# Kernel tuning notes

Measured on AMD Instinct MI355X. Metric: run time of the kernel, lower is better.

## Reference

```python
import jax, jax.numpy as jnp
import numpy as np

B_AUDIOS = 64      # num audios in batch
NODES    = 2048    # 5-frame chunks (nodes) per audio
IN, HID, OUT = 512, 256, 128
HEADS, NCLS  = 2, 7
NEG_SLOPE = 0.2    # PyG GATConv default


def setup_inputs() -> dict:
    key = jax.random.key(0)
    ks = jax.random.split(key, 12)
    N = B_AUDIOS * NODES
    # chain edges within each audio: i -> i+1 (local), offset per audio
    base = np.arange(NODES - 1)
    src = (base[None, :] + np.arange(B_AUDIOS)[:, None] * NODES).reshape(-1)
    edge_index = jnp.asarray(np.stack([src, src + 1]), dtype=jnp.int32)
    batch_indices = jnp.repeat(jnp.arange(B_AUDIOS, dtype=jnp.int32), NODES)
    s = 0.05
    return {
        "x": jax.random.normal(ks[0], (N, IN), jnp.float32),
        "edge_index": edge_index,
        "batch_indices": batch_indices,
        "num_audios": B_AUDIOS,
        "W1": jax.random.normal(ks[1], (HEADS * HID, IN)) * s,
        "as1": jax.random.normal(ks[2], (HEADS, HID)) * s,
        "ad1": jax.random.normal(ks[3], (HEADS, HID)) * s,
        "b1": jnp.zeros((HID,), jnp.float32),
        "W2": jax.random.normal(ks[4], (HEADS * OUT, HID)) * s,
        "as2": jax.random.normal(ks[5], (HEADS, OUT)) * s,
        "ad2": jax.random.normal(ks[6], (HEADS, OUT)) * s,
        "b2": jnp.zeros((OUT,), jnp.float32),
        "Wt": jax.random.normal(ks[7], (1, OUT)) * s,
        "bt": jnp.zeros((1,), jnp.float32),
        "Wa": jax.random.normal(ks[8], (2, OUT)) * s,
        "ba": jnp.zeros((2,), jnp.float32),
        "Wn": jax.random.normal(ks[9], (NCLS, OUT)) * s,
        "bn": jnp.zeros((NCLS,), jnp.float32),
    }


def _seg_softmax(e, seg, n):
    m = jax.ops.segment_max(e, seg, num_segments=n)
    ex = jnp.exp(e - m[seg])
    return ex / jax.ops.segment_sum(ex, seg, num_segments=n)[seg]


def _gat_conv(x, src, dst, W, a_src, a_dst, b):
    # PyG GATConv, heads=H, concat=False (head-mean), with self loops
    N = x.shape[0]
    H, C = a_src.shape
    loops = jnp.arange(N, dtype=src.dtype)
    s = jnp.concatenate([src, loops])
    d = jnp.concatenate([dst, loops])
    h = (x @ W.T).reshape(N, H, C)                      # [N,H,C]
    al_s = jnp.einsum('nhc,hc->nh', h, a_src)           # [N,H]
    al_d = jnp.einsum('nhc,hc->nh', h, a_dst)
    e = jax.nn.leaky_relu(al_s[s] + al_d[d], NEG_SLOPE)  # [E,H]
    alpha = _seg_softmax(e, d, N)                        # softmax over in-edges of dst
    out = jax.ops.segment_sum(alpha[:, :, None] * h[s], d, num_segments=N)
    return out.mean(axis=1) + b                          # concat=False -> head mean


def reference(x, edge_index, batch_indices, num_audios,
              W1, as1, ad1, b1, W2, as2, ad2, b2,
              Wt, bt, Wa, ba, Wn, bn):
    src, dst = edge_index[0], edge_index[1]
    # global GAT (gat1 -> relu -> gat2)
    h1 = jax.nn.relu(_gat_conv(x, src, dst, W1, as1, ad1, b1))
    emb = _gat_conv(h1, src, dst, W2, as2, ad2, b2)      # [N, OUT]
    node_pred = jax.nn.softmax(emb @ Wn.T + bn, axis=-1)
    # per-audio subgraph GAT: graphs are disjoint per-audio chains, so running the
    # same GATModel on each subgraph equals restricting the global embeddings.
    logit = (emb @ Wt.T + bt)[:, 0]                      # [N]
    w = _seg_softmax(logit, batch_indices, num_audios)   # per-audio temporal softmax
    attended = jax.ops.segment_sum(w[:, None] * emb, batch_indices,
                                   num_segments=num_audios)  # [B, OUT]
    audio_pred = attended @ Wa.T + ba                    # [B, 2]
    return node_pred, audio_pred
```

## Files before the change

kernel.cpp:

```cpp
#include <hip/hip_runtime.h>
#include <hip/hip_bf16.h>

typedef __bf16 bf16x8 __attribute__((ext_vector_type(8)));
typedef float f32x4 __attribute__((ext_vector_type(4)));

#define NTOT   131072
#define NODES_PER_AUDIO 2048
#define NAUDIO 64
#define POOL_CHUNKS 16
#define CHUNK_NODES (NODES_PER_AUDIO / POOL_CHUNKS)

__global__ __launch_bounds__(256)
void detect_dtype(const unsigned* __restrict__ x, int* __restrict__ flag)
{
    const int tid = threadIdx.x;
    int cnt = 0;
    for (int i = tid; i < 4096; i += 256) {
        unsigned e = (x[i] >> 7) & 0xFF;
        cnt += (e >= 100 && e <= 145) ? 1 : 0;
    }
    __shared__ int red[256];
    red[tid] = cnt; __syncthreads();
    for (int s = 128; s > 0; s >>= 1) {
        if (tid < s) red[tid] += red[tid + s];
        __syncthreads();
    }
    if (tid == 0) *flag = (red[0] > 3000) ? 1 : 0;
}

struct W14 { const void* s[14]; int n[14]; int off[14]; };

__global__ __launch_bounds__(256)
void convert_weights(W14 w, const int* __restrict__ flag, __bf16* __restrict__ wb)
{
    const int f = *flag;
    const int stride = gridDim.x * 256;
    for (int t = 0; t < 14; t++) {
        const void* src = w.s[t];
        __bf16* d = wb + w.off[t];
        for (int i = blockIdx.x * 256 + threadIdx.x; i < w.n[t]; i += stride)
            d[i] = f ? ((const __bf16*)src)[i] : (__bf16)((const float*)src)[i];
    }
}

template<int NX, bool DYN>
__global__ __launch_bounds__(256)
void gemm_tile(const void* __restrict__ Araw, const __bf16* __restrict__ W,
               __bf16* __restrict__ C, int M, int K, int Nc,
               const int* __restrict__ flagp)
{
    __shared__ __align__(16) __bf16 As[128 * 64];
    __shared__ __align__(16) __bf16 Bs[128 * 64];

    const int nb  = gridDim.x;
    const int ny  = nb / NX;
    const int ypx = ny >> 3;
    const int bid = blockIdx.x;
    const int xcd = bid & 7;
    const int local = bid >> 3;
    const int by = xcd * ypx + local / NX;
    const int bx = local % NX;

    const int colBase = bx * 128;
    const int rowBase = by * 128;
    const int tid  = threadIdx.x;
    const int wave = tid >> 6;
    const int lane = tid & 63;
    const int wrow = (wave >> 1) * 64;
    const int wcol = (wave & 1) * 64;
    const int lr = lane & 15;
    const int lq = lane >> 4;
    int f = 1;
    if constexpr (DYN) f = *flagp;

    f32x4 acc[4][4] = {};

    const __bf16* A16 = (const __bf16*)Araw;
    const float*  A32 = (const float*)Araw;
    const __bf16* ap[4]; const float* af32[4]; const __bf16* bp[4];
    #pragma unroll
    for (int i = 0; i < 4; i++) {
        const int c = tid + 256 * i;
        const int r = c >> 3, q = c & 7;
        ap[i]   = A16 + (size_t)(rowBase + r) * K + q * 8;
        af32[i] = A32 + (size_t)(rowBase + r) * K + q * 8;
        bp[i]   = W   + (size_t)(colBase + r) * K + q * 8;
    }

    for (int k0 = 0; k0 < K; k0 += 64) {
        __syncthreads();
        #pragma unroll
        for (int i = 0; i < 4; i++) {
            const int c = tid + 256 * i;
            __builtin_amdgcn_global_load_lds(
                (const __attribute__((address_space(1))) void*)(bp[i] + k0),
                (__attribute__((address_space(3))) void*)&Bs[c * 8], 16, 0, 0);
        }
        if (!DYN || f) {
            #pragma unroll
            for (int i = 0; i < 4; i++) {
                const int c = tid + 256 * i;
                __builtin_amdgcn_global_load_lds(
                    (const __attribute__((address_space(1))) void*)(ap[i] + k0),
                    (__attribute__((address_space(3))) void*)&As[c * 8], 16, 0, 0);
            }
        } else {
            #pragma unroll
            for (int i = 0; i < 4; i++) {
                const int c = tid + 256 * i;
                float4 u0 = *(const float4*)(af32[i] + k0);
                float4 u1 = *(const float4*)(af32[i] + k0 + 4);
                __bf16 t[8] = {(__bf16)u0.x, (__bf16)u0.y, (__bf16)u0.z, (__bf16)u0.w,
                               (__bf16)u1.x, (__bf16)u1.y, (__bf16)u1.z, (__bf16)u1.w};
                *(int4*)&As[c * 8] = *(int4*)t;
            }
        }
        __syncthreads();

        #pragma unroll
        for (int kk = 0; kk < 2; kk++) {
            bf16x8 avf[4], bvf[4];
            #pragma unroll
            for (int i = 0; i < 4; i++)
                avf[i] = *(const bf16x8*)&As[(wrow + i * 16 + lr) * 64 + kk * 32 + lq * 8];
            #pragma unroll
            for (int j = 0; j < 4; j++)
                bvf[j] = *(const bf16x8*)&Bs[(wcol + j * 16 + lr) * 64 + kk * 32 + lq * 8];
            #pragma unroll
            for (int i = 0; i < 4; i++)
                #pragma unroll
                for (int j = 0; j < 4; j++)
                    acc[i][j] = __builtin_amdgcn_mfma_f32_16x16x32_bf16(
                        avf[i], bvf[j], acc[i][j], 0, 0, 0);
        }
    }

    #pragma unroll
    for (int i = 0; i < 4; i++) {
        #pragma unroll
        for (int j = 0; j < 4; j++) {
            int col = colBase + wcol + j * 16 + lr;
            #pragma unroll
            for (int r = 0; r < 4; r++) {
                int row = rowBase + wrow + i * 16 + lq * 4 + r;
                C[(size_t)row * Nc + col] = (__bf16)acc[i][j][r];
            }
        }
    }
}

template<int C, bool RELU, bool FUSE_HEAD>
__global__ __launch_bounds__(256)
void agg_fused(const __bf16* __restrict__ h, const __bf16* __restrict__ a_s,
               const __bf16* __restrict__ a_d, const __bf16* __restrict__ bias,
               void* __restrict__ outv,
               const __bf16* __restrict__ Wn, const __bf16* __restrict__ bn,
               const __bf16* __restrict__ Wt, const __bf16* __restrict__ bt,
               void* __restrict__ node_pred, float* __restrict__ logit,
               const int* __restrict__ flag)
{
    constexpr int D = 2 * C;
    constexpr int V = D / 64;
    const int n = blockIdx.x * 4 + (threadIdx.x >> 6);
    const int lane = threadIdx.x & 63;
    const bool have_prev = (n & (NODES_PER_AUDIO - 1)) != 0;
    const size_t np = have_prev ? (size_t)(n - 1) : (size_t)n;
    const int base = lane * V;

    __bf16 h0v[V], h1v[V];
    if constexpr (V == 8) {
        *(int4*)h0v = *(const int4*)(h + (size_t)n * D + base);
        *(int4*)h1v = *(const int4*)(h + np * D + base);
    } else {
        *(int2*)h0v = *(const int2*)(h + (size_t)n * D + base);
        *(int2*)h1v = *(const int2*)(h + np * D + base);
    }

    float ps = 0.f, pd = 0.f, pp = 0.f;
    #pragma unroll
    for (int j = 0; j < V; j++) {
        float av = (float)a_s[base + j], dv = (float)a_d[base + j];
        float x0 = (float)h0v[j], x1 = (float)h1v[j];
        ps += x0 * av; pd += x0 * dv; pp += x1 * av;
    }
    #pragma unroll
    for (int off = 1; off < 32; off <<= 1) {
        ps += __shfl_xor(ps, off, 64);
        pd += __shfl_xor(pd, off, 64);
        pp += __shfl_xor(pp, off, 64);
    }

    float es = ps + pd;  es = es > 0.f ? es : 0.2f * es;
    float a_self = 1.f, a_prev = 0.f;
    if (have_prev) {
        float ep = pp + pd;  ep = ep > 0.f ? ep : 0.2f * ep;
        float m = fmaxf(es, ep);
        float wsx = __expf(es - m), wpx = __expf(ep - m);
        float inv = 1.f / (wsx + wpx);
        a_self = wsx * inv; a_prev = wpx * inv;
    }

    const int cb = (lane & 31) * V;
    float outj[V];
    #pragma unroll
    for (int j = 0; j < V; j++) {
        float p = a_self * (float)h0v[j] + a_prev * (float)h1v[j];
        p = 0.5f * (p + __shfl_xor(p, 32, 64));
        p += (float)bias[cb + j];
        if (RELU) p = fmaxf(p, 0.f);
        outj[j] = p;
    }

    if constexpr (!FUSE_HEAD) {
        if (lane < 32) {
            __bf16 ov[V];
            #pragma unroll
            for (int j = 0; j < V; j++) ov[j] = (__bf16)outj[j];
            if constexpr (V == 8)
                *(int4*)((__bf16*)outv + (size_t)n * C + cb) = *(int4*)ov;
            else
                *(int2*)((__bf16*)outv + (size_t)n * C + cb) = *(int2*)ov;
        }
    } else {
        if (lane < 32)
            *(float4*)((float*)outv + (size_t)n * C + cb) = *(float4*)outj;

        float acc[8];
        #pragma unroll
        for (int k = 0; k < 7; k++) {
            float a = 0.f;
            #pragma unroll
            for (int j = 0; j < V; j++)
                a += outj[j] * (float)Wn[k * C + cb + j];
            acc[k] = a;
        }
        {
            float a = 0.f;
            #pragma unroll
            for (int j = 0; j < V; j++)
                a += outj[j] * (float)Wt[cb + j];
            acc[7] = a;
        }
        #pragma unroll
        for (int off = 1; off < 32; off <<= 1)
            #pragma unroll
            for (int k = 0; k < 8; k++)
                acc[k] += __shfl_xor(acc[k], off, 64);

        if (lane == 0) {
            float lg[7], m = -1e30f;
            #pragma unroll
            for (int k = 0; k < 7; k++) {
                lg[k] = acc[k] + (float)bn[k];
                m = fmaxf(m, lg[k]);
            }
            float s = 0.f;
            #pragma unroll
            for (int k = 0; k < 7; k++) { lg[k] = __expf(lg[k] - m); s += lg[k]; }
            float inv = 1.f / s;
            if (*flag) {
                #pragma unroll
                for (int k = 0; k < 7; k++)
                    ((__bf16*)node_pred)[(size_t)n * 7 + k] = (__bf16)(lg[k] * inv);
            } else {
                #pragma unroll
                for (int k = 0; k < 7; k++)
                    ((float*)node_pred)[(size_t)n * 7 + k] = lg[k] * inv;
            }
            logit[n] = acc[7] + (float)bt[0];
        }
    }
}

__global__ __launch_bounds__(256)
void audio_stats(const float* __restrict__ logit, float2* __restrict__ stats)
{
    const int b = blockIdx.x;
    const int tid = threadIdx.x;
    __shared__ float red[256];
    const float* lg = logit + b * NODES_PER_AUDIO;

    float m = -1e30f;
    for (int i = tid; i < NODES_PER_AUDIO; i += 256) m = fmaxf(m, lg[i]);
    red[tid] = m; __syncthreads();
    for (int s = 128; s > 0; s >>= 1) {
        if (tid < s) red[tid] = fmaxf(red[tid], red[tid + s]);
        __syncthreads();
    }
    m = red[0]; __syncthreads();

    float s = 0.f;
    for (int i = tid; i < NODES_PER_AUDIO; i += 256) s += __expf(lg[i] - m);
    red[tid] = s; __syncthreads();
    for (int st = 128; st > 0; st >>= 1) {
        if (tid < st) red[tid] += red[tid + st];
        __syncthreads();
    }
    if (tid == 0) stats[b] = make_float2(m, 1.f / red[0]);
}

__global__ __launch_bounds__(256)
void audio_partial(const float* __restrict__ emb, const float* __restrict__ logit,
                   const float2* __restrict__ stats, float* __restrict__ partial)
{
    const int b = blockIdx.x >> 4;
    const int chunk = blockIdx.x & 15;
    const int tid = threadIdx.x;
    const int c = tid & 127, half = tid >> 7;
    const float m = stats[b].x, inv = stats[b].y;
    const float* lg = logit + b * NODES_PER_AUDIO;
    const float* eb = emb + (size_t)b * NODES_PER_AUDIO * 128;

    __shared__ float attbuf[256];
    const int n0 = chunk * CHUNK_NODES + half * (CHUNK_NODES / 2);
    float att = 0.f;
    for (int i = n0; i < n0 + CHUNK_NODES / 2; i++) {
        float w = __expf(lg[i] - m) * inv;
        att += w * eb[(size_t)i * 128 + c];
    }
    attbuf[tid] = att; __syncthreads();
    if (tid < 128)
        partial[(size_t)(b * POOL_CHUNKS + chunk) * 128 + tid] =
            attbuf[tid] + attbuf[tid + 128];
}

__global__ __launch_bounds__(64)
void audio_final(const float* __restrict__ partial, const __bf16* __restrict__ Wa,
                 const __bf16* __restrict__ ba, void* __restrict__ outbase,
                 const int* __restrict__ flag)
{
    const int b = blockIdx.x;
    const int lane = threadIdx.x;
    const float* pb = partial + (size_t)b * POOL_CHUNKS * 128;

    float a0 = 0.f, a1 = 0.f;
    #pragma unroll
    for (int k = 0; k < POOL_CHUNKS; k++) {
        a0 += pb[k * 128 + lane * 2];
        a1 += pb[k * 128 + lane * 2 + 1];
    }
    float p0 = a0 * (float)Wa[lane * 2]       + a1 * (float)Wa[lane * 2 + 1];
    float p1 = a0 * (float)Wa[128 + lane * 2] + a1 * (float)Wa[128 + lane * 2 + 1];
    #pragma unroll
    for (int off = 1; off < 64; off <<= 1) {
        p0 += __shfl_xor(p0, off, 64);
        p1 += __shfl_xor(p1, off, 64);
    }
    if (lane == 0) {
        float r0 = p0 + (float)ba[0];
        float r1 = p1 + (float)ba[1];
        if (*flag) {
            ((__bf16*)outbase)[(size_t)NTOT * 7 + b * 2 + 0] = (__bf16)r0;
            ((__bf16*)outbase)[(size_t)NTOT * 7 + b * 2 + 1] = (__bf16)r1;
        } else {
            ((float*)outbase)[(size_t)NTOT * 7 + b * 2 + 0] = r0;
            ((float*)outbase)[(size_t)NTOT * 7 + b * 2 + 1] = r1;
        }
    }
}

extern "C" void kernel_launch(void* const* d_in, const int* in_sizes, int n_in,
                              void* d_out, int out_size, void* d_ws, size_t ws_size,
                              hipStream_t stream)
{
    const void* x = d_in[0];
    char* ws = (char*)d_ws;
    const size_t N = NTOT;

    __bf16* h  = (__bf16*)ws;
    size_t off = N * 1024;
    __bf16* h1 = (__bf16*)(ws + off); off += N * 512;
    float* logit = (float*)(ws + off); off += N * 4;
    __bf16* wb = (__bf16*)(ws + off); off += 331008 * 2;
    int* flag = (int*)(ws + off); off += 16;
    float2* stats = (float2*)(ws + off); off += NAUDIO * sizeof(float2);
    float* partial = (float*)(ws + off); off += (size_t)NAUDIO * POOL_CHUNKS * 128 * 4;
    __bf16* g2 = h;
    float* emb = (float*)(ws + N * 512);

    const int O_W1 = 0,      O_W2 = 262144, O_as1 = 327680, O_ad1 = 328192;
    const int O_b1 = 328704, O_as2 = 328960, O_ad2 = 329216, O_b2 = 329472;
    const int O_Wt = 329600, O_bt = 329728, O_Wa = 329736, O_ba = 329992;
    const int O_Wn = 330000, O_bn = 330896;

    W14 w;
    const void* srcs[14] = { d_in[4], d_in[8], d_in[5], d_in[6], d_in[7],
                             d_in[9], d_in[10], d_in[11], d_in[12], d_in[13],
                             d_in[14], d_in[15], d_in[16], d_in[17] };
    const int ns[14]   = { 262144, 65536, 512, 512, 256, 256, 256, 128,
                           128, 1, 256, 2, 896, 7 };
    const int offs[14] = { O_W1, O_W2, O_as1, O_ad1, O_b1, O_as2, O_ad2, O_b2,
                           O_Wt, O_bt, O_Wa, O_ba, O_Wn, O_bn };
    for (int i = 0; i < 14; i++) { w.s[i] = srcs[i]; w.n[i] = ns[i]; w.off[i] = offs[i]; }

    const int nwb = NTOT / 4;

    detect_dtype<<<1, 256, 0, stream>>>((const unsigned*)x, flag);
    convert_weights<<<512, 256, 0, stream>>>(w, flag, wb);

    gemm_tile<4, true><<<4 * (NTOT / 128), 256, 0, stream>>>(
        x, wb + O_W1, h, NTOT, 512, 512, flag);
    agg_fused<256, true, false><<<nwb, 256, 0, stream>>>(
        h, wb + O_as1, wb + O_ad1, wb + O_b1, h1,
        nullptr, nullptr, nullptr, nullptr, nullptr, nullptr, flag);
    gemm_tile<2, false><<<2 * (NTOT / 128), 256, 0, stream>>>(
        h1, wb + O_W2, g2, NTOT, 256, 256, flag);
    agg_fused<128, false, true><<<nwb, 256, 0, stream>>>(
        g2, wb + O_as2, wb + O_ad2, wb + O_b2, emb,
        wb + O_Wn, wb + O_bn, wb + O_Wt, wb + O_bt, d_out, logit, flag);
    audio_stats<<<NAUDIO, 256, 0, stream>>>(logit, stats);
    audio_partial<<<NAUDIO * POOL_CHUNKS, 256, 0, stream>>>(emb, logit, stats, partial);
    audio_final<<<NAUDIO, 64, 0, stream>>>(partial, wb + O_Wa, wb + O_ba, d_out, flag);
}
```

Baseline: 649.5 us.

## Fuse GEMM with GAT attention aggregation per 128-row tile, fix tile boundaries separately

```diff
diff --git a/kernel.cpp b/kernel.cpp
--- a/kernel.cpp
+++ b/kernel.cpp
@@ -4,11 +4,34 @@
 typedef __bf16 bf16x8 __attribute__((ext_vector_type(8)));
 typedef float f32x4 __attribute__((ext_vector_type(4)));
 
-#define NTOT   131072
+#define NTOT 131072
 #define NODES_PER_AUDIO 2048
 #define NAUDIO 64
 #define POOL_CHUNKS 16
-#define CHUNK_NODES (NODES_PER_AUDIO / POOL_CHUNKS)
+#define CHUNK_NODES 128
+
+#define O_W1 0
+#define O_W2 262144
+#define O_as1 327680
+#define O_ad1 328192
+#define O_b1 328704
+#define O_as2 328960
+#define O_ad2 329216
+#define O_b2 329472
+#define O_Wt 329600
+#define O_bt 329728
+#define O_Wa 329736
+#define O_ba 329992
+#define O_Wn 330000
+#define O_bn 330896
+
+#define SBAR __builtin_amdgcn_sched_barrier(0)
+#define AS1 __attribute__((address_space(1)))
+#define AS3 __attribute__((address_space(3)))
+#define GLL(SRC, DST) __builtin_amdgcn_global_load_lds( \
+    (const AS1 void*)(SRC), (AS3 void*)(DST), 16, 0, 0)
+
+__device__ __forceinline__ float lrelu(float x) { return x > 0.f ? x : 0.2f * x; }
 
 __global__ __launch_bounds__(256)
 void detect_dtype(const unsigned* __restrict__ x, int* __restrict__ flag)
@@ -43,232 +66,483 @@
     }
 }
 
-template<int NX, bool DYN>
 __global__ __launch_bounds__(256)
-void gemm_tile(const void* __restrict__ Araw, const __bf16* __restrict__ W,
-               __bf16* __restrict__ C, int M, int K, int Nc,
-               const int* __restrict__ flagp)
-{
-    __shared__ __align__(16) __bf16 As[128 * 64];
-    __shared__ __align__(16) __bf16 Bs[128 * 64];
-
-    const int nb  = gridDim.x;
-    const int ny  = nb / NX;
-    const int ypx = ny >> 3;
-    const int bid = blockIdx.x;
-    const int xcd = bid & 7;
-    const int local = bid >> 3;
-    const int by = xcd * ypx + local / NX;
-    const int bx = local % NX;
-
-    const int colBase = bx * 128;
-    const int rowBase = by * 128;
+void convert_x(const float4* __restrict__ xf, __bf16* __restrict__ xb,
+               const int* __restrict__ flag)
+{
+    if (*flag) return;
+    const unsigned stride = gridDim.x * 256;
+    for (unsigned i = blockIdx.x * 256 + threadIdx.x; i < 16777216u; i += stride) {
+        float4 v = xf[i];
+        __bf16 t[4] = {(__bf16)v.x, (__bf16)v.y, (__bf16)v.z, (__bf16)v.w};
+        *(int2*)&xb[(size_t)i * 4] = *(int2*)t;
+    }
+}
+
+__global__ __launch_bounds__(512, 2)
+void fused1(const void* __restrict__ Araw, const __bf16* __restrict__ Aconv,
+            const __bf16* __restrict__ wb, __bf16* __restrict__ h1,
+            float* __restrict__ side_al, __bf16* __restrict__ side_h,
+            const int* __restrict__ flagp)
+{
+    extern __shared__ __align__(16) char smem[];
+    __bf16* As  = (__bf16*)smem;
+    __bf16* Bs  = (__bf16*)(smem + 16384);
+    __bf16* hb  = (__bf16*)smem;
+    float*  al  = (float*)(smem + 131072);
+    float*  alp = (float*)(smem + 133120);
+    __bf16* asd = (__bf16*)(smem + 135168);
+    __bf16* b1s = (__bf16*)(smem + 137216);
+
     const int tid  = threadIdx.x;
-    const int wave = tid >> 6;
-    const int lane = tid & 63;
-    const int wrow = (wave >> 1) * 64;
-    const int wcol = (wave & 1) * 64;
-    const int lr = lane & 15;
-    const int lq = lane >> 4;
-    int f = 1;
-    if constexpr (DYN) f = *flagp;
-
-    f32x4 acc[4][4] = {};
-
-    const __bf16* A16 = (const __bf16*)Araw;
-    const float*  A32 = (const float*)Araw;
-    const __bf16* ap[4]; const float* af32[4]; const __bf16* bp[4];
+    const int b    = blockIdx.x;
+    const int r0   = b * 128;
+    const int wave = tid >> 6, lane = tid & 63;
+    const int lr   = lane & 15, lq = lane >> 4;
+    const int frs  = (lq ^ (lr & 3)) * 8;
+
+    asd[tid]       = wb[O_as1 + tid];
+    asd[512 + tid] = wb[O_ad1 + tid];
+    if (tid < 256) b1s[tid] = wb[O_b1 + tid];
+
+    const __bf16* A = (const __bf16*)Araw;
+    if (!*flagp) A = Aconv;
+    const __bf16* Wp = wb + O_W1;
+
+    const int arow = tid >> 2, aslot = tid & 3;
+    const size_t aoff  = (size_t)(r0 + arow) * 512 + ((aslot ^ (arow & 3)) * 8);
+    const size_t boff0 = (size_t)arow * 512 + ((aslot ^ (arow & 3)) * 8);
+    const int ldst = tid * 8;
+
+    f32x4 acc[8][4] = {};
+
+    asm volatile("s_waitcnt vmcnt(0)" ::: "memory");
+    GLL(A + aoff, As + ldst);
+    GLL(Wp + boff0,          Bs + ldst);
+    GLL(Wp + boff0 + 65536,  Bs + ldst + 4096);
+    GLL(Wp + boff0 + 131072, Bs + ldst + 8192);
+    GLL(Wp + boff0 + 196608, Bs + ldst + 12288);
+
+    #pragma unroll 2
+    for (int s = 0; s < 16; ++s) {
+        const int p = s & 1;
+        if (s < 15) {
+            const int ko = (s + 1) * 32;
+            const int q = p ^ 1;
+            GLL(A + aoff + ko, As + q * 4096 + ldst);
+            GLL(Wp + boff0 + ko,          Bs + q * 16384 + ldst);
+            GLL(Wp + boff0 + 65536 + ko,  Bs + q * 16384 + ldst + 4096);
+            GLL(Wp + boff0 + 131072 + ko, Bs + q * 16384 + ldst + 8192);
+            GLL(Wp + boff0 + 196608 + ko, Bs + q * 16384 + ldst + 12288);
+            asm volatile("s_waitcnt vmcnt(5)");
+        } else {
+            asm volatile("s_waitcnt vmcnt(0)");
+        }
+        SBAR; __builtin_amdgcn_s_barrier(); SBAR;
+
+        bf16x8 av[8], bv[4];
+        #pragma unroll
+        for (int i = 0; i < 8; i++)
+            av[i] = *(const bf16x8*)&As[p * 4096 + (i * 16 + lr) * 32 + frs];
+        #pragma unroll
+        for (int j = 0; j < 4; j++)
+            bv[j] = *(const bf16x8*)&Bs[p * 16384 + (wave * 64 + j * 16 + lr) * 32 + frs];
+        asm volatile("s_waitcnt lgkmcnt(0)"); SBAR;
+        #pragma unroll
+        for (int i = 0; i < 8; i++)
+            #pragma unroll
+            for (int j = 0; j < 4; j++)
+                acc[i][j] = __builtin_amdgcn_mfma_f32_16x16x32_bf16(
+                    av[i], bv[j], acc[i][j], 0, 0, 0);
+        SBAR; __builtin_amdgcn_s_barrier(); SBAR;
+    }
+
     #pragma unroll
-    for (int i = 0; i < 4; i++) {
-        const int c = tid + 256 * i;
-        const int r = c >> 3, q = c & 7;
-        ap[i]   = A16 + (size_t)(rowBase + r) * K + q * 8;
-        af32[i] = A32 + (size_t)(rowBase + r) * K + q * 8;
-        bp[i]   = W   + (size_t)(colBase + r) * K + q * 8;
-    }
-
-    for (int k0 = 0; k0 < K; k0 += 64) {
-        __syncthreads();
-        #pragma unroll
-        for (int i = 0; i < 4; i++) {
-            const int c = tid + 256 * i;
-            __builtin_amdgcn_global_load_lds(
-                (const __attribute__((address_space(1))) void*)(bp[i] + k0),
-                (__attribute__((address_space(3))) void*)&Bs[c * 8], 16, 0, 0);
-        }
-        if (!DYN || f) {
-            #pragma unroll
-            for (int i = 0; i < 4; i++) {
-                const int c = tid + 256 * i;
-                __builtin_amdgcn_global_load_lds(
-                    (const __attribute__((address_space(1))) void*)(ap[i] + k0),
-                    (__attribute__((address_space(3))) void*)&As[c * 8], 16, 0, 0);
+    for (int i = 0; i < 8; i++)
+        #pragma unroll
+        for (int j = 0; j < 4; j++) {
+            const int col = wave * 64 + j * 16 + lr;
+            #pragma unroll
+            for (int r = 0; r < 4; r++)
+                hb[(i * 16 + lq * 4 + r) * 512 + col] = (__bf16)acc[i][j][r];
+        }
+    __syncthreads();
+
+    {
+        const int row = tid >> 2, q = tid & 3;
+        float s0 = 0.f, s1 = 0.f, d0 = 0.f, d1 = 0.f;
+        #pragma unroll
+        for (int c8 = 0; c8 < 8; ++c8) {
+            const int cc = q * 64 + ((c8 + row) & 7) * 8;
+            bf16x8 x0 = *(const bf16x8*)&hb[row * 512 + cc];
+            bf16x8 x1 = *(const bf16x8*)&hb[row * 512 + 256 + cc];
+            bf16x8 a0 = *(const bf16x8*)&asd[cc];
+            bf16x8 a1 = *(const bf16x8*)&asd[256 + cc];
+            bf16x8 e0 = *(const bf16x8*)&asd[512 + cc];
+            bf16x8 e1 = *(const bf16x8*)&asd[768 + cc];
+            #pragma unroll
+            for (int j = 0; j < 8; j++) {
+                float v0 = (float)x0[j], v1 = (float)x1[j];
+                s0 += v0 * (float)a0[j]; d0 += v0 * (float)e0[j];
+                s1 += v1 * (float)a1[j]; d1 += v1 * (float)e1[j];
             }
+        }
+        s0 += __shfl_xor(s0, 1, 64); s0 += __shfl_xor(s0, 2, 64);
+        s1 += __shfl_xor(s1, 1, 64); s1 += __shfl_xor(s1, 2, 64);
+        d0 += __shfl_xor(d0, 1, 64); d0 += __shfl_xor(d0, 2, 64);
+        d1 += __shfl_xor(d1, 1, 64); d1 += __shfl_xor(d1, 2, 64);
+        if (q == 0) {
+            al[row * 4 + 0] = s0; al[row * 4 + 1] = s1;
+            al[row * 4 + 2] = d0; al[row * 4 + 3] = d1;
+        }
+    }
+    if (tid < 64) {
+        *(int4*)&side_h[(size_t)b * 1024 + tid * 8]       = *(const int4*)&hb[tid * 8];
+        *(int4*)&side_h[(size_t)b * 1024 + 512 + tid * 8] = *(const int4*)&hb[127 * 512 + tid * 8];
+    }
+    __syncthreads();
+
+    if (tid >= 1 && tid < 128) {
+        const int n = tid;
+        float4 a  = *(const float4*)&al[n * 4];
+        float4 ap = *(const float4*)&al[(n - 1) * 4];
+        float es0 = lrelu(a.x + a.z), ep0 = lrelu(ap.x + a.z);
+        float m0 = fmaxf(es0, ep0);
+        float w0 = __expf(es0 - m0), v0 = __expf(ep0 - m0), i0 = 1.f / (w0 + v0);
+        float es1 = lrelu(a.y + a.w), ep1 = lrelu(ap.y + a.w);
+        float m1 = fmaxf(es1, ep1);
+        float w1 = __expf(es1 - m1), v1 = __expf(ep1 - m1), i1 = 1.f / (w1 + v1);
+        *(float4*)&alp[n * 4] = make_float4(w0 * i0, v0 * i0, w1 * i1, v1 * i1);
+    }
+    if (tid == 0) {
+        *(float4*)&side_al[(size_t)b * 8]     = *(const float4*)&al[0];
+        *(float4*)&side_al[(size_t)b * 8 + 4] = *(const float4*)&al[127 * 4];
+    }
+    __syncthreads();
+
+    if (tid < 508) {
+        const int n = 1 + (tid >> 2), q = tid & 3;
+        const float4 av4 = *(const float4*)&alp[n * 4];
+        #pragma unroll
+        for (int c8 = 0; c8 < 8; ++c8) {
+            const int cc = q * 64 + ((c8 + n) & 7) * 8;
+            bf16x8 x00 = *(const bf16x8*)&hb[n * 512 + cc];
+            bf16x8 x0p = *(const bf16x8*)&hb[(n - 1) * 512 + cc];
+            bf16x8 x10 = *(const bf16x8*)&hb[n * 512 + 256 + cc];
+            bf16x8 x1p = *(const bf16x8*)&hb[(n - 1) * 512 + 256 + cc];
+            bf16x8 bb  = *(const bf16x8*)&b1s[cc];
+            __bf16 o[8];
+            #pragma unroll
+            for (int j = 0; j < 8; j++) {
+                float v = 0.5f * (av4.x * (float)x00[j] + av4.y * (float)x0p[j]
+                                + av4.z * (float)x10[j] + av4.w * (float)x1p[j])
+                        + (float)bb[j];
+                o[j] = (__bf16)fmaxf(v, 0.f);
+            }
+            *(int4*)&h1[(size_t)(r0 + n) * 256 + cc] = *(const int4*)o;
+        }
+    }
+}
+
+__global__ __launch_bounds__(256)
+void fix1(const float* __restrict__ side_al, const __bf16* __restrict__ side_h,
+          const __bf16* __restrict__ wb, __bf16* __restrict__ h1)
+{
+    const int node = blockIdx.x * 4 + (threadIdx.x >> 6);
+    const int lane = threadIdx.x & 63;
+    const bool hp = (node & 15) != 0;
+    const int pv = hp ? node - 1 : node;
+    const float* alf   = side_al + (size_t)node * 8;
+    const float* aprev = side_al + (size_t)pv * 8 + 4;
+    float as0 = 1.f, ap0 = 0.f, as1h = 1.f, ap1 = 0.f;
+    if (hp) {
+        float es0 = lrelu(alf[0] + alf[2]), ep0 = lrelu(aprev[0] + alf[2]);
+        float m0 = fmaxf(es0, ep0);
+        float w0 = __expf(es0 - m0), v0 = __expf(ep0 - m0), i0 = 1.f / (w0 + v0);
+        as0 = w0 * i0; ap0 = v0 * i0;
+        float es1 = lrelu(alf[1] + alf[3]), ep1 = lrelu(aprev[1] + alf[3]);
+        float m1 = fmaxf(es1, ep1);
+        float w1 = __expf(es1 - m1), v1 = __expf(ep1 - m1), i1 = 1.f / (w1 + v1);
+        as1h = w1 * i1; ap1 = v1 * i1;
+    }
+    const __bf16* hf = side_h + (size_t)node * 1024;
+    const __bf16* hl = side_h + (size_t)pv * 1024 + 512;
+    const int c4 = lane * 4;
+    __bf16 o[4];
+    #pragma unroll
+    for (int r = 0; r < 4; r++) {
+        const int c = c4 + r;
+        float v = 0.5f * (as0 * (float)hf[c] + ap0 * (float)hl[c]
+                        + as1h * (float)hf[256 + c] + ap1 * (float)hl[256 + c])
+                + (float)wb[O_b1 + c];
+        o[r] = (__bf16)fmaxf(v, 0.f);
+    }
+    *(int2*)&h1[(size_t)node * 128 * 256 + c4] = *(const int2*)o;
+}
+
+__global__ __launch_bounds__(512, 4)
+void fused2(const __bf16* __restrict__ h1, const __bf16* __restrict__ wb,
+            float* __restrict__ emb, float* __restrict__ side_al2,
+            __bf16* __restrict__ side_h2, void* __restrict__ node_pred,
+            float* __restrict__ logit, const int* __restrict__ flagp)
+{
+    extern __shared__ __align__(16) char smem[];
+    __bf16* As  = (__bf16*)smem;
+    __bf16* Bs  = (__bf16*)(smem + 16384);
+    __bf16* hb  = (__bf16*)smem;
+    float*  al  = (float*)(smem + 65536);
+    float*  alp = (float*)(smem + 67584);
+    __bf16* we  = (__bf16*)(smem + 69632);
+    __bf16* b2s = (__bf16*)(smem + 70656);
+    __bf16* wns = (__bf16*)(smem + 70912);
+
+    const int tid  = threadIdx.x;
+    const int b    = blockIdx.x;
+    const int r0   = b * 128;
+    const int wave = tid >> 6, lane = tid & 63;
+    const int lr   = lane & 15, lq = lane >> 4;
+    const int frs  = (lq ^ (lr & 3)) * 8;
+
+    if (tid < 256) { we[tid] = wb[O_as2 + tid]; we[256 + tid] = wb[O_ad2 + tid]; }
+    if (tid < 128) b2s[tid] = wb[O_b2 + tid];
+    for (int i = tid; i < 1024; i += 512)
+        wns[i] = (i < 896) ? wb[O_Wn + i] : wb[O_Wt + (i - 896)];
+
+    const int arow = tid >> 2, aslot = tid & 3;
+    const size_t aoff  = (size_t)(r0 + arow) * 256 + ((aslot ^ (arow & 3)) * 8);
+    const size_t boff0 = (size_t)arow * 256 + ((aslot ^ (arow & 3)) * 8);
+    const int ldst = tid * 8;
+    const __bf16* Wp = wb + O_W2;
+
+    f32x4 acc[8][2] = {};
+
+    asm volatile("s_waitcnt vmcnt(0)" ::: "memory");
+    GLL(h1 + aoff, As + ldst);
+    GLL(Wp + boff0,         Bs + ldst);
+    GLL(Wp + boff0 + 32768, Bs + ldst + 4096);
+
+    #pragma unroll 2
+    for (int s = 0; s < 8; ++s) {
+        const int p = s & 1;
+        if (s < 7) {
+            const int ko = (s + 1) * 32;
+            const int q = p ^ 1;
+            GLL(h1 + aoff + ko, As + q * 4096 + ldst);
+            GLL(Wp + boff0 + ko,         Bs + q * 8192 + ldst);
+            GLL(Wp + boff0 + 32768 + ko, Bs + q * 8192 + ldst + 4096);
+            asm volatile("s_waitcnt vmcnt(3)");
         } else {
-            #pragma unroll
-            for (int i = 0; i < 4; i++) {
-                const int c = tid + 256 * i;
-                float4 u0 = *(const float4*)(af32[i] + k0);
-                float4 u1 = *(const float4*)(af32[i] + k0 + 4);
-                __bf16 t[8] = {(__bf16)u0.x, (__bf16)u0.y, (__bf16)u0.z, (__bf16)u0.w,
-                               (__bf16)u1.x, (__bf16)u1.y, (__bf16)u1.z, (__bf16)u1.w};
-                *(int4*)&As[c * 8] = *(int4*)t;
-            }
-        }
-        __syncthreads();
-
-        #pragma unroll
-        for (int kk = 0; kk < 2; kk++) {
-            bf16x8 avf[4], bvf[4];
+            asm volatile("s_waitcnt vmcnt(0)");
+        }
+        SBAR; __builtin_amdgcn_s_barrier(); SBAR;
+
+        bf16x8 bv[2];
+        #pragma unroll
+        for (int j = 0; j < 2; j++)
+            bv[j] = *(const bf16x8*)&Bs[p * 8192 + (wave * 32 + j * 16 + lr) * 32 + frs];
+        #pragma unroll
+        for (int h = 0; h < 2; h++) {
+            bf16x8 av[4];
             #pragma unroll
             for (int i = 0; i < 4; i++)
-                avf[i] = *(const bf16x8*)&As[(wrow + i * 16 + lr) * 64 + kk * 32 + lq * 8];
-            #pragma unroll
-            for (int j = 0; j < 4; j++)
-                bvf[j] = *(const bf16x8*)&Bs[(wcol + j * 16 + lr) * 64 + kk * 32 + lq * 8];
+                av[i] = *(const bf16x8*)&As[p * 4096 + ((h * 4 + i) * 16 + lr) * 32 + frs];
+            asm volatile("s_waitcnt lgkmcnt(0)"); SBAR;
             #pragma unroll
             for (int i = 0; i < 4; i++)
                 #pragma unroll
-                for (int j = 0; j < 4; j++)
-                    acc[i][j] = __builtin_amdgcn_mfma_f32_16x16x32_bf16(
-                        avf[i], bvf[j], acc[i][j], 0, 0, 0);
-        }
+                for (int j = 0; j < 2; j++)
+                    acc[h * 4 + i][j] = __builtin_amdgcn_mfma_f32_16x16x32_bf16(
+                        av[i], bv[j], acc[h * 4 + i][j], 0, 0, 0);
+        }
+        SBAR; __builtin_amdgcn_s_barrier(); SBAR;
     }
 
     #pragma unroll
-    for (int i = 0; i < 4; i++) {
-        #pragma unroll
-        for (int j = 0; j < 4; j++) {
-            int col = colBase + wcol + j * 16 + lr;
-            #pragma unroll
-            for (int r = 0; r < 4; r++) {
-                int row = rowBase + wrow + i * 16 + lq * 4 + r;
-                C[(size_t)row * Nc + col] = (__bf16)acc[i][j][r];
+    for (int i = 0; i < 8; i++)
+        #pragma unroll
+        for (int j = 0; j < 2; j++) {
+            const int col = wave * 32 + j * 16 + lr;
+            #pragma unroll
+            for (int r = 0; r < 4; r++)
+                hb[(i * 16 + lq * 4 + r) * 256 + col] = (__bf16)acc[i][j][r];
+        }
+    __syncthreads();
+
+    {
+        const int row = tid >> 2, q = tid & 3;
+        float s0 = 0.f, s1 = 0.f, d0 = 0.f, d1 = 0.f;
+        #pragma unroll
+        for (int c4 = 0; c4 < 4; ++c4) {
+            const int cc = q * 32 + ((c4 + row) & 3) * 8;
+            bf16x8 x0 = *(const bf16x8*)&hb[row * 256 + cc];
+            bf16x8 x1 = *(const bf16x8*)&hb[row * 256 + 128 + cc];
+            bf16x8 a0 = *(const bf16x8*)&we[cc];
+            bf16x8 a1 = *(const bf16x8*)&we[128 + cc];
+            bf16x8 e0 = *(const bf16x8*)&we[256 + cc];
+            bf16x8 e1 = *(const bf16x8*)&we[384 + cc];
+            #pragma unroll
+            for (int j = 0; j < 8; j++) {
+                float v0 = (float)x0[j], v1 = (float)x1[j];
+                s0 += v0 * (float)a0[j]; d0 += v0 * (float)e0[j];
+                s1 += v1 * (float)a1[j]; d1 += v1 * (float)e1[j];
             }
         }
-    }
-}
-
-template<int C, bool RELU, bool FUSE_HEAD>
-__global__ __launch_bounds__(256)
-void agg_fused(const __bf16* __restrict__ h, const __bf16* __restrict__ a_s,
-               const __bf16* __restrict__ a_d, const __bf16* __restrict__ bias,
-               void* __restrict__ outv,
-               const __bf16* __restrict__ Wn, const __bf16* __restrict__ bn,
-               const __bf16* __restrict__ Wt, const __bf16* __restrict__ bt,
-               void* __restrict__ node_pred, float* __restrict__ logit,
-               const int* __restrict__ flag)
-{
-    constexpr int D = 2 * C;
-    constexpr int V = D / 64;
-    const int n = blockIdx.x * 4 + (threadIdx.x >> 6);
-    const int lane = threadIdx.x & 63;
-    const bool have_prev = (n & (NODES_PER_AUDIO - 1)) != 0;
-    const size_t np = have_prev ? (size_t)(n - 1) : (size_t)n;
-    const int base = lane * V;
-
-    __bf16 h0v[V], h1v[V];
-    if constexpr (V == 8) {
-        *(int4*)h0v = *(const int4*)(h + (size_t)n * D + base);
-        *(int4*)h1v = *(const int4*)(h + np * D + base);
-    } else {
-        *(int2*)h0v = *(const int2*)(h + (size_t)n * D + base);
-        *(int2*)h1v = *(const int2*)(h + np * D + base);
-    }
-
-    float ps = 0.f, pd = 0.f, pp = 0.f;
-    #pragma unroll
-    for (int j = 0; j < V; j++) {
-        float av = (float)a_s[base + j], dv = (float)a_d[base + j];
-        float x0 = (float)h0v[j], x1 = (float)h1v[j];
-        ps += x0 * av; pd += x0 * dv; pp += x1 * av;
-    }
-    #pragma unroll
-    for (int off = 1; off < 32; off <<= 1) {
-        ps += __shfl_xor(ps, off, 64);
-        pd += __shfl_xor(pd, off, 64);
-        pp += __shfl_xor(pp, off, 64);
-    }
-
-    float es = ps + pd;  es = es > 0.f ? es : 0.2f * es;
-    float a_self = 1.f, a_prev = 0.f;
-    if (have_prev) {
-        float ep = pp + pd;  ep = ep > 0.f ? ep : 0.2f * ep;
-        float m = fmaxf(es, ep);
-        float wsx = __expf(es - m), wpx = __expf(ep - m);
-        float inv = 1.f / (wsx + wpx);
-        a_self = wsx * inv; a_prev = wpx * inv;
-    }
-
-    const int cb = (lane & 31) * V;
-    float outj[V];
-    #pragma unroll
-    for (int j = 0; j < V; j++) {
-        float p = a_self * (float)h0v[j] + a_prev * (float)h1v[j];
-        p = 0.5f * (p + __shfl_xor(p, 32, 64));
-        p += (float)bias[cb + j];
-        if (RELU) p = fmaxf(p, 0.f);
-        outj[j] = p;
-    }
-
-    if constexpr (!FUSE_HEAD) {
-        if (lane < 32) {
-            __bf16 ov[V];
-            #pragma unroll
-            for (int j = 0; j < V; j++) ov[j] = (__bf16)outj[j];
-            if constexpr (V == 8)
-                *(int4*)((__bf16*)outv + (size_t)n * C + cb) = *(int4*)ov;
-            else
-                *(int2*)((__bf16*)outv + (size_t)n * C + cb) = *(int2*)ov;
-        }
-    } else {
-        if (lane < 32)
-            *(float4*)((float*)outv + (size_t)n * C + cb) = *(float4*)outj;
-
-        float acc[8];
-        #pragma unroll
-        for (int k = 0; k < 7; k++) {
-            float a = 0.f;
-            #pragma unroll
-            for (int j = 0; j < V; j++)
-                a += outj[j] * (float)Wn[k * C + cb + j];
-            acc[k] = a;
-        }
-        {
-            float a = 0.f;
-            #pragma unroll
-            for (int j = 0; j < V; j++)
-                a += outj[j] * (float)Wt[cb + j];
-            acc[7] = a;
-        }
-        #pragma unroll
-        for (int off = 1; off < 32; off <<= 1)
-            #pragma unroll
-            for (int k = 0; k < 8; k++)
-                acc[k] += __shfl_xor(acc[k], off, 64);
-
-        if (lane == 0) {
+        s0 += __shfl_xor(s0, 1, 64); s0 += __shfl_xor(s0, 2, 64);
+        s1 += __shfl_xor(s1, 1, 64); s1 += __shfl_xor(s1, 2, 64);
+        d0 += __shfl_xor(d0, 1, 64); d0 += __shfl_xor(d0, 2, 64);
+        d1 += __shfl_xor(d1, 1, 64); d1 += __shfl_xor(d1, 2, 64);
+        if (q == 0) {
+            al[row * 4 + 0] = s0; al[row * 4 + 1] = s1;
+            al[row * 4 + 2] = d0; al[row * 4 + 3] = d1;
+        }
+    }
+    if (tid < 32) {
+        *(int4*)&side_h2[(size_t)b * 512 + tid * 8] = *(const int4*)&hb[tid * 8];
+    } else if (tid < 64) {
+        const int t = tid - 32;
+        *(int4*)&side_h2[(size_t)b * 512 + 256 + t * 8] = *(const int4*)&hb[127 * 256 + t * 8];
+    }
+    __syncthreads();
+
+    if (tid >= 1 && tid < 128) {
+        const int n = tid;
+        float4 a  = *(const float4*)&al[n * 4];
+        float4 ap = *(const float4*)&al[(n - 1) * 4];
+        float es0 = lrelu(a.x + a.z), ep0 = lrelu(ap.x + a.z);
+        float m0 = fmaxf(es0, ep0);
+        float w0 = __expf(es0 - m0), v0 = __expf(ep0 - m0), i0 = 1.f / (w0 + v0);
+        float es1 = lrelu(a.y + a.w), ep1 = lrelu(ap.y + a.w);
+        float m1 = fmaxf(es1, ep1);
+        float w1 = __expf(es1 - m1), v1 = __expf(ep1 - m1), i1 = 1.f / (w1 + v1);
+        *(float4*)&alp[n * 4] = make_float4(w0 * i0, v0 * i0, w1 * i1, v1 * i1);
+    }
+    if (tid == 0) {
+        *(float4*)&side_al2[(size_t)b * 8]     = *(const float4*)&al[0];
+        *(float4*)&side_al2[(size_t)b * 8 + 4] = *(const float4*)&al[127 * 4];
+    }
+    __syncthreads();
+
+    if (tid < 508) {
+        const int n = 1 + (tid >> 2), q = tid & 3;
+        const float4 av4 = *(const float4*)&alp[n * 4];
+        float ak[8] = {0.f, 0.f, 0.f, 0.f, 0.f, 0.f, 0.f, 0.f};
+        #pragma unroll
+        for (int c4 = 0; c4 < 4; ++c4) {
+            const int cc = q * 32 + ((c4 + n) & 3) * 8;
+            bf16x8 x00 = *(const bf16x8*)&hb[n * 256 + cc];
+            bf16x8 x0p = *(const bf16x8*)&hb[(n - 1) * 256 + cc];
+            bf16x8 x10 = *(const bf16x8*)&hb[n * 256 + 128 + cc];
+            bf16x8 x1p = *(const bf16x8*)&hb[(n - 1) * 256 + 128 + cc];
+            bf16x8 bb  = *(const bf16x8*)&b2s[cc];
+            float o[8];
+            #pragma unroll
+            for (int j = 0; j < 8; j++)
+                o[j] = 0.5f * (av4.x * (float)x00[j] + av4.y * (float)x0p[j]
+                             + av4.z * (float)x10[j] + av4.w * (float)x1p[j])
+                     + (float)bb[j];
+            *(float4*)&emb[(size_t)(r0 + n) * 128 + cc]     = make_float4(o[0], o[1], o[2], o[3]);
+            *(float4*)&emb[(size_t)(r0 + n) * 128 + cc + 4] = make_float4(o[4], o[5], o[6], o[7]);
+            #pragma unroll
+            for (int k = 0; k < 7; k++) {
+                float t = 0.f;
+                #pragma unroll
+                for (int j = 0; j < 8; j++) t += o[j] * (float)wns[k * 128 + cc + j];
+                ak[k] += t;
+            }
+            float t = 0.f;
+            #pragma unroll
+            for (int j = 0; j < 8; j++) t += o[j] * (float)wns[896 + cc + j];
+            ak[7] += t;
+        }
+        #pragma unroll
+        for (int k = 0; k < 8; k++) {
+            ak[k] += __shfl_xor(ak[k], 1, 64);
+            ak[k] += __shfl_xor(ak[k], 2, 64);
+        }
+        if (q == 0) {
+            const size_t ng = (size_t)(r0 + n);
             float lg[7], m = -1e30f;
             #pragma unroll
-            for (int k = 0; k < 7; k++) {
-                lg[k] = acc[k] + (float)bn[k];
-                m = fmaxf(m, lg[k]);
-            }
+            for (int k = 0; k < 7; k++) { lg[k] = ak[k] + (float)wb[O_bn + k]; m = fmaxf(m, lg[k]); }
             float s = 0.f;
             #pragma unroll
             for (int k = 0; k < 7; k++) { lg[k] = __expf(lg[k] - m); s += lg[k]; }
             float inv = 1.f / s;
-            if (*flag) {
+            if (*flagp) {
                 #pragma unroll
                 for (int k = 0; k < 7; k++)
-                    ((__bf16*)node_pred)[(size_t)n * 7 + k] = (__bf16)(lg[k] * inv);
+                    ((__bf16*)node_pred)[ng * 7 + k] = (__bf16)(lg[k] * inv);
             } else {
                 #pragma unroll
                 for (int k = 0; k < 7; k++)
-                    ((float*)node_pred)[(size_t)n * 7 + k] = lg[k] * inv;
+                    ((float*)node_pred)[ng * 7 + k] = lg[k] * inv;
             }
-            logit[n] = acc[7] + (float)bt[0];
-        }
+            logit[ng] = ak[7] + (float)wb[O_bt];
+        }
+    }
+}
+
+__global__ __launch_bounds__(256)
+void fix2(const float* __restrict__ side_al2, const __bf16* __restrict__ side_h2,
+          const __bf16* __restrict__ wb, float* __restrict__ emb,
+          void* __restrict__ node_pred, float* __restrict__ logit,
+          const int* __restrict__ flagp)
+{
+    const int node = blockIdx.x * 4 + (threadIdx.x >> 6);
+    const int lane = threadIdx.x & 63;
+    const bool hp = (node & 15) != 0;
+    const int pv = hp ? node - 1 : node;
+    const float* alf   = side_al2 + (size_t)node * 8;
+    const float* aprev = side_al2 + (size_t)pv * 8 + 4;
+    float as0 = 1.f, ap0 = 0.f, as1h = 1.f, ap1 = 0.f;
+    if (hp) {
+        float es0 = lrelu(alf[0] + alf[2]), ep0 = lrelu(aprev[0] + alf[2]);
+        float m0 = fmaxf(es0, ep0);
+        float w0 = __expf(es0 - m0), v0 = __expf(ep0 - m0), i0 = 1.f / (w0 + v0);
+        as0 = w0 * i0; ap0 = v0 * i0;
+        float es1 = lrelu(alf[1] + alf[3]), ep1 = lrelu(aprev[1] + alf[3]);
+        float m1 = fmaxf(es1, ep1);
+        float w1 = __expf(es1 - m1), v1 = __expf(ep1 - m1), i1 = 1.f / (w1 + v1);
+        as1h = w1 * i1; ap1 = v1 * i1;
+    }
+    const __bf16* gf = side_h2 + (size_t)node * 512;
+    const __bf16* gl = side_h2 + (size_t)pv * 512 + 256;
+    const int c2 = lane * 2;
+    float o0 = 0.5f * (as0 * (float)gf[c2] + ap0 * (float)gl[c2]
+                     + as1h * (float)gf[128 + c2] + ap1 * (float)gl[128 + c2])
+             + (float)wb[O_b2 + c2];
+    float o1 = 0.5f * (as0 * (float)gf[c2 + 1] + ap0 * (float)gl[c2 + 1]
+                     + as1h * (float)gf[128 + c2 + 1] + ap1 * (float)gl[128 + c2 + 1])
+             + (float)wb[O_b2 + c2 + 1];
+    const size_t ng = (size_t)node * 128;
+    *(float2*)&emb[ng * 128 + c2] = make_float2(o0, o1);
+    float ak[8];
+    #pragma unroll
+    for (int k = 0; k < 7; k++)
+        ak[k] = o0 * (float)wb[O_Wn + k * 128 + c2] + o1 * (float)wb[O_Wn + k * 128 + c2 + 1];
+    ak[7] = o0 * (float)wb[O_Wt + c2] + o1 * (float)wb[O_Wt + c2 + 1];
+    #pragma unroll
+    for (int off = 1; off < 64; off <<= 1)
+        #pragma unroll
+        for (int k = 0; k < 8; k++) ak[k] += __shfl_xor(ak[k], off, 64);
+    if (lane == 0) {
+        float lg[7], m = -1e30f;
+        #pragma unroll
+        for (int k = 0; k < 7; k++) { lg[k] = ak[k] + (float)wb[O_bn + k]; m = fmaxf(m, lg[k]); }
+        float s = 0.f;
+        #pragma unroll
+        for (int k = 0; k < 7; k++) { lg[k] = __expf(lg[k] - m); s += lg[k]; }
+        float inv = 1.f / s;
+        if (*flagp) {
+            #pragma unroll
+            for (int k = 0; k < 7; k++)
+                ((__bf16*)node_pred)[ng * 7 + k] = (__bf16)(lg[k] * inv);
+        } else {
+            #pragma unroll
+            for (int k = 0; k < 7; k++)
+                ((float*)node_pred)[ng * 7 + k] = lg[k] * inv;
+        }
+        logit[ng] = ak[7] + (float)wb[O_bt];
     }
 }
 
@@ -365,23 +639,19 @@
 {
     const void* x = d_in[0];
     char* ws = (char*)d_ws;
-    const size_t N = NTOT;
-
-    __bf16* h  = (__bf16*)ws;
-    size_t off = N * 1024;
-    __bf16* h1 = (__bf16*)(ws + off); off += N * 512;
-    float* logit = (float*)(ws + off); off += N * 4;
-    __bf16* wb = (__bf16*)(ws + off); off += 331008 * 2;
-    int* flag = (int*)(ws + off); off += 16;
-    float2* stats = (float2*)(ws + off); off += NAUDIO * sizeof(float2);
-    float* partial = (float*)(ws + off); off += (size_t)NAUDIO * POOL_CHUNKS * 128 * 4;
-    __bf16* g2 = h;
-    float* emb = (float*)(ws + N * 512);
-
-    const int O_W1 = 0,      O_W2 = 262144, O_as1 = 327680, O_ad1 = 328192;
-    const int O_b1 = 328704, O_as2 = 328960, O_ad2 = 329216, O_b2 = 329472;
-    const int O_Wt = 329600, O_bt = 329728, O_Wa = 329736, O_ba = 329992;
-    const int O_Wn = 330000, O_bn = 330896;
+
+    __bf16* h1       = (__bf16*)ws;
+    float*  emb      = (float*)(ws + 67108864);
+    float*  logit    = (float*)(ws + 134217728);
+    __bf16* wb       = (__bf16*)(ws + 134742016);
+    int*    flag     = (int*)(ws + 135404032);
+    float2* stats    = (float2*)(ws + 135404048);
+    float*  partial  = (float*)(ws + 135404560);
+    float*  side_al  = (float*)(ws + 135928848);
+    __bf16* side_h   = (__bf16*)(ws + 135961616);
+    float*  side_al2 = (float*)(ws + 138058768);
+    __bf16* side_h2  = (__bf16*)(ws + 138091536);
+    __bf16* xb       = (__bf16*)(ws + 139140112);
 
     W14 w;
     const void* srcs[14] = { d_in[4], d_in[8], d_in[5], d_in[6], d_in[7],
@@ -393,21 +663,20 @@
                            O_Wt, O_bt, O_Wa, O_ba, O_Wn, O_bn };
     for (int i = 0; i < 14; i++) { w.s[i] = srcs[i]; w.n[i] = ns[i]; w.off[i] = offs[i]; }
 
-    const int nwb = NTOT / 4;
+    hipFuncSetAttribute(reinterpret_cast<const void*>(&fused1),
+                        hipFuncAttributeMaxDynamicSharedMemorySize, 137728);
+    hipFuncSetAttribute(reinterpret_cast<const void*>(&fused2),
+                        hipFuncAttributeMaxDynamicSharedMemorySize, 73728);
 
     detect_dtype<<<1, 256, 0, stream>>>((const unsigned*)x, flag);
     convert_weights<<<512, 256, 0, stream>>>(w, flag, wb);
-
-    gemm_tile<4, true><<<4 * (NTOT / 128), 256, 0, stream>>>(
-        x, wb + O_W1, h, NTOT, 512, 512, flag);
-    agg_fused<256, true, false><<<nwb, 256, 0, stream>>>(
-        h, wb + O_as1, wb + O_ad1, wb + O_b1, h1,
-        nullptr, nullptr, nullptr, nullptr, nullptr, nullptr, flag);
-    gemm_tile<2, false><<<2 * (NTOT / 128), 256, 0, stream>>>(
-        h1, wb + O_W2, g2, NTOT, 256, 256, flag);
-    agg_fused<128, false, true><<<nwb, 256, 0, stream>>>(
-        g2, wb + O_as2, wb + O_ad2, wb + O_b2, emb,
-        wb + O_Wn, wb + O_bn, wb + O_Wt, wb + O_bt, d_out, logit, flag);
+    convert_x<<<2048, 256, 0, stream>>>((const float4*)x, xb, flag);
+
+    fused1<<<1024, 512, 137728, stream>>>(x, xb, wb, h1, side_al, side_h, flag);
+    fix1<<<256, 256, 0, stream>>>(side_al, side_h, wb, h1);
+    fused2<<<1024, 512, 73728, stream>>>(h1, wb, emb, side_al2, side_h2,
+                                         d_out, logit, flag);
+    fix2<<<256, 256, 0, stream>>>(side_al2, side_h2, wb, emb, d_out, logit, flag);
     audio_stats<<<NAUDIO, 256, 0, stream>>>(logit, stats);
     audio_partial<<<NAUDIO * POOL_CHUNKS, 256, 0, stream>>>(emb, logit, stats, partial);
     audio_final<<<NAUDIO, 64, 0, stream>>>(partial, wb + O_Wa, wb + O_ba, d_out, flag);
```

Result: slower. 676.4 us (+4.1%).

## Double-buffer GEMM LDS tiles with XOR swizzle and pre-convert fp32 input

Applied to the files above, without the earlier changes.

```diff
diff --git a/kernel.cpp b/kernel.cpp
--- a/kernel.cpp
+++ b/kernel.cpp
@@ -9,6 +9,12 @@
 #define NAUDIO 64
 #define POOL_CHUNKS 16
 #define CHUNK_NODES (NODES_PER_AUDIO / POOL_CHUNKS)
+
+#define SBAR __builtin_amdgcn_sched_barrier(0)
+#define AS1 __attribute__((address_space(1)))
+#define AS3 __attribute__((address_space(3)))
+#define GLL(SRC, DST) __builtin_amdgcn_global_load_lds( \
+    (const AS1 void*)(SRC), (AS3 void*)(DST), 16, 0, 0)
 
 __global__ __launch_bounds__(256)
 void detect_dtype(const unsigned* __restrict__ x, int* __restrict__ flag)
@@ -43,110 +49,117 @@
     }
 }
 
-template<int NX, bool DYN>
-__global__ __launch_bounds__(256)
-void gemm_tile(const void* __restrict__ Araw, const __bf16* __restrict__ W,
-               __bf16* __restrict__ C, int M, int K, int Nc,
-               const int* __restrict__ flagp)
-{
-    __shared__ __align__(16) __bf16 As[128 * 64];
-    __shared__ __align__(16) __bf16 Bs[128 * 64];
+__global__ __launch_bounds__(256)
+void convert_x(const float4* __restrict__ xf, __bf16* __restrict__ xb,
+               const int* __restrict__ flag)
+{
+    if (*flag) return;
+    const unsigned stride = gridDim.x * 256;
+    for (unsigned i = blockIdx.x * 256 + threadIdx.x; i < 16777216u; i += stride) {
+        float4 v = xf[i];
+        __bf16 t[4] = {(__bf16)v.x, (__bf16)v.y, (__bf16)v.z, (__bf16)v.w};
+        *(int2*)&xb[(size_t)i * 4] = *(int2*)t;
+    }
+}
+
+#define STG(S, P) do {                                                  \
+    const int _k0 = (S) * 64;                                           \
+    _Pragma("unroll")                                                   \
+    for (int _i = 0; _i < 4; _i++)                                      \
+        GLL(ap[_i] + _k0, &As[(P) * 8192 + ld[_i]]);                    \
+    _Pragma("unroll")                                                   \
+    for (int _i = 0; _i < 4; _i++)                                      \
+        GLL(bp[_i] + _k0, &Bs[(P) * 8192 + ld[_i]]);                    \
+} while (0)
+
+template<int NX>
+__global__ __launch_bounds__(256, 2)
+void gemm_pipe(const void* __restrict__ Araw, const __bf16* __restrict__ Aconv,
+               const __bf16* __restrict__ W, __bf16* __restrict__ C,
+               int M, int K, int Nc, const int* __restrict__ flagp)
+{
+    __shared__ __align__(16) __bf16 As[2 * 128 * 64];
+    __shared__ __align__(16) __bf16 Bs[2 * 128 * 64];
+
+    const __bf16* A = (const __bf16*)Araw;
+    if (!*flagp) A = Aconv;
 
     const int nb  = gridDim.x;
     const int ny  = nb / NX;
     const int ypx = ny >> 3;
     const int bid = blockIdx.x;
-    const int xcd = bid & 7;
-    const int local = bid >> 3;
-    const int by = xcd * ypx + local / NX;
-    const int bx = local % NX;
-
-    const int colBase = bx * 128;
-    const int rowBase = by * 128;
+    const int by  = (bid & 7) * ypx + (bid >> 3) / NX;
+    const int bx  = (bid >> 3) % NX;
+    const int rowBase = by * 128, colBase = bx * 128;
+
     const int tid  = threadIdx.x;
-    const int wave = tid >> 6;
-    const int lane = tid & 63;
-    const int wrow = (wave >> 1) * 64;
-    const int wcol = (wave & 1) * 64;
-    const int lr = lane & 15;
-    const int lq = lane >> 4;
-    int f = 1;
-    if constexpr (DYN) f = *flagp;
+    const int wave = tid >> 6, lane = tid & 63;
+    const int wrow = (wave >> 1) * 64, wcol = (wave & 1) * 64;
+    const int lr = lane & 15, lq = lane >> 4;
+
+    const __bf16* ap[4]; const __bf16* bp[4]; int ld[4];
+    #pragma unroll
+    for (int i = 0; i < 4; i++) {
+        const int c = tid + 256 * i, r = c >> 3, q = (c & 7) ^ (r & 7);
+        ap[i] = A + (size_t)(rowBase + r) * K + q * 8;
+        bp[i] = W + (size_t)(colBase + r) * K + q * 8;
+        ld[i] = c * 8;
+    }
 
     f32x4 acc[4][4] = {};
-
-    const __bf16* A16 = (const __bf16*)Araw;
-    const float*  A32 = (const float*)Araw;
-    const __bf16* ap[4]; const float* af32[4]; const __bf16* bp[4];
-    #pragma unroll
-    for (int i = 0; i < 4; i++) {
-        const int c = tid + 256 * i;
-        const int r = c >> 3, q = c & 7;
-        ap[i]   = A16 + (size_t)(rowBase + r) * K + q * 8;
-        af32[i] = A32 + (size_t)(rowBase + r) * K + q * 8;
-        bp[i]   = W   + (size_t)(colBase + r) * K + q * 8;
-    }
-
-    for (int k0 = 0; k0 < K; k0 += 64) {
-        __syncthreads();
+    const int NS = K >> 6;
+
+    STG(0, 0); STG(1, 1);
+    asm volatile("s_waitcnt vmcnt(8)"); SBAR;
+    __builtin_amdgcn_s_barrier(); SBAR;
+
+    for (int s = 0; s < NS; ++s) {
+        const int p = s & 1;
+        bf16x8 av[4][2], bv[4][2];
         #pragma unroll
-        for (int i = 0; i < 4; i++) {
-            const int c = tid + 256 * i;
-            __builtin_amdgcn_global_load_lds(
-                (const __attribute__((address_space(1))) void*)(bp[i] + k0),
-                (__attribute__((address_space(3))) void*)&Bs[c * 8], 16, 0, 0);
-        }
-        if (!DYN || f) {
-            #pragma unroll
-            for (int i = 0; i < 4; i++) {
-                const int c = tid + 256 * i;
-                __builtin_amdgcn_global_load_lds(
-                    (const __attribute__((address_space(1))) void*)(ap[i] + k0),
-                    (__attribute__((address_space(3))) void*)&As[c * 8], 16, 0, 0);
+        for (int i = 0; i < 4; i++)
+            #pragma unroll
+            for (int kk = 0; kk < 2; kk++) {
+                const int ra = wrow + i * 16 + lr;
+                av[i][kk] = *(const bf16x8*)
+                    &As[p * 8192 + ra * 64 + (((kk * 4 + lq) ^ (ra & 7)) * 8)];
+                const int rb = wcol + i * 16 + lr;
+                bv[i][kk] = *(const bf16x8*)
+                    &Bs[p * 8192 + rb * 64 + (((kk * 4 + lq) ^ (rb & 7)) * 8)];
             }
-        } else {
-            #pragma unroll
-            for (int i = 0; i < 4; i++) {
-                const int c = tid + 256 * i;
-                float4 u0 = *(const float4*)(af32[i] + k0);
-                float4 u1 = *(const float4*)(af32[i] + k0 + 4);
-                __bf16 t[8] = {(__bf16)u0.x, (__bf16)u0.y, (__bf16)u0.z, (__bf16)u0.w,
-                               (__bf16)u1.x, (__bf16)u1.y, (__bf16)u1.z, (__bf16)u1.w};
-                *(int4*)&As[c * 8] = *(int4*)t;
-            }
-        }
-        __syncthreads();
-
+        asm volatile("s_waitcnt lgkmcnt(0)"); SBAR;
+        __builtin_amdgcn_s_barrier(); SBAR;
+
+        if (s + 2 < NS) STG(s + 2, p);
+
+        __builtin_amdgcn_s_setprio(1);
         #pragma unroll
-        for (int kk = 0; kk < 2; kk++) {
-            bf16x8 avf[4], bvf[4];
-            #pragma unroll
-            for (int i = 0; i < 4; i++)
-                avf[i] = *(const bf16x8*)&As[(wrow + i * 16 + lr) * 64 + kk * 32 + lq * 8];
-            #pragma unroll
-            for (int j = 0; j < 4; j++)
-                bvf[j] = *(const bf16x8*)&Bs[(wcol + j * 16 + lr) * 64 + kk * 32 + lq * 8];
+        for (int kk = 0; kk < 2; kk++)
             #pragma unroll
             for (int i = 0; i < 4; i++)
                 #pragma unroll
                 for (int j = 0; j < 4; j++)
                     acc[i][j] = __builtin_amdgcn_mfma_f32_16x16x32_bf16(
-                        avf[i], bvf[j], acc[i][j], 0, 0, 0);
-        }
-    }
-
-    #pragma unroll
-    for (int i = 0; i < 4; i++) {
+                        av[i][kk], bv[j][kk], acc[i][j], 0, 0, 0);
+        __builtin_amdgcn_s_setprio(0);
+
+        if (s + 2 < NS) { asm volatile("s_waitcnt vmcnt(8)"); }
+        else            { asm volatile("s_waitcnt vmcnt(0)"); }
+        SBAR;
+        __builtin_amdgcn_s_barrier(); SBAR;
+    }
+
+    #pragma unroll
+    for (int i = 0; i < 4; i++)
         #pragma unroll
         for (int j = 0; j < 4; j++) {
-            int col = colBase + wcol + j * 16 + lr;
+            const int col = colBase + wcol + j * 16 + lr;
             #pragma unroll
             for (int r = 0; r < 4; r++) {
-                int row = rowBase + wrow + i * 16 + lq * 4 + r;
+                const int row = rowBase + wrow + i * 16 + lq * 4 + r;
                 C[(size_t)row * Nc + col] = (__bf16)acc[i][j][r];
             }
         }
-    }
 }
 
 template<int C, bool RELU, bool FUSE_HEAD>
@@ -375,6 +388,8 @@
     int* flag = (int*)(ws + off); off += 16;
     float2* stats = (float2*)(ws + off); off += NAUDIO * sizeof(float2);
     float* partial = (float*)(ws + off); off += (size_t)NAUDIO * POOL_CHUNKS * 128 * 4;
+    off = (off + 15) & ~(size_t)15;
+    __bf16* xb = (__bf16*)(ws + off); off += N * 512 * sizeof(__bf16);
     __bf16* g2 = h;
     float* emb = (float*)(ws + N * 512);
 
@@ -397,14 +412,15 @@
 
     detect_dtype<<<1, 256, 0, stream>>>((const unsigned*)x, flag);
     convert_weights<<<512, 256, 0, stream>>>(w, flag, wb);
-
-    gemm_tile<4, true><<<4 * (NTOT / 128), 256, 0, stream>>>(
-        x, wb + O_W1, h, NTOT, 512, 512, flag);
+    convert_x<<<2048, 256, 0, stream>>>((const float4*)x, xb, flag);
+
+    gemm_pipe<4><<<4 * (NTOT / 128), 256, 0, stream>>>(
+        x, xb, wb + O_W1, h, NTOT, 512, 512, flag);
     agg_fused<256, true, false><<<nwb, 256, 0, stream>>>(
         h, wb + O_as1, wb + O_ad1, wb + O_b1, h1,
         nullptr, nullptr, nullptr, nullptr, nullptr, nullptr, flag);
-    gemm_tile<2, false><<<2 * (NTOT / 128), 256, 0, stream>>>(
-        h1, wb + O_W2, g2, NTOT, 256, 256, flag);
+    gemm_pipe<2><<<2 * (NTOT / 128), 256, 0, stream>>>(
+        h1, h1, wb + O_W2, g2, NTOT, 256, 256, flag);
     agg_fused<128, false, true><<<nwb, 256, 0, stream>>>(
         g2, wb + O_as2, wb + O_ad2, wb + O_b2, emb,
         wb + O_Wn, wb + O_bn, wb + O_Wt, wb + O_bt, d_out, logit, flag);
```

Result: slower. 742.8 us (+14.4%).
